# Kernel tuning notes

Hardware: AMD Instinct MI355X
Metric: run time of the kernel (lower is better)

Reference implementation:

```python
import jax, jax.numpy as jnp
import numpy as np

B, S, D, H, L = 8, 512, 1024, 16, 2
DH = D // H
EPS = 1e-6
SCALE = float(np.sqrt(DH))


def _ln(x, g, b):
    # custom LayerNormalization: unbiased std (torch default), eps added to std
    m = x.mean(axis=-1, keepdims=True)
    s = jnp.std(x, axis=-1, keepdims=True, ddof=1)
    return g * (x - m) / (s + EPS) + b


def _pos_encoding(seq_len, dim):
    pos = jnp.arange(seq_len, dtype=jnp.float32)[:, None]
    dims = jnp.arange(dim, dtype=jnp.float32)
    div = 10000.0 ** (2.0 * dims / dim)
    pe = jnp.zeros((seq_len, dim), jnp.float32)
    pe = pe.at[:, 0::2].set(jnp.sin(pos / div[0::2]))
    pe = pe.at[:, 1::2].set(jnp.cos(pos / div[1::2]))
    return pe


def setup_inputs() -> dict:
    key = jax.random.key(0)
    ks = jax.random.split(key, 20)
    std = 0.02
    p = lambda k, shape: jax.random.normal(k, shape, jnp.float32) * std
    return {
        "features": jax.random.normal(ks[0], (B, S, D), jnp.float32),
        "mask": jnp.ones((B, S), jnp.int32),
        "ln_in_g": jnp.ones((D,), jnp.float32),
        "ln_in_b": jnp.zeros((D,), jnp.float32),
        "Wq": p(ks[1], (L, D, D)), "bq": p(ks[2], (L, D)),
        "Wk": p(ks[3], (L, D, D)), "bk": p(ks[4], (L, D)),
        "Wv": p(ks[5], (L, D, D)), "bv": p(ks[6], (L, D)),
        "Wo": p(ks[7], (L, D, D)), "bo": p(ks[8], (L, D)),
        "ln1_g": jnp.ones((L, D), jnp.float32), "ln1_b": jnp.zeros((L, D), jnp.float32),
        "W1": p(ks[9], (L, D, D)), "b1": p(ks[10], (L, D)),
        "W2": p(ks[11], (L, D, D)), "b2": p(ks[12], (L, D)),
        "ln2_g": jnp.ones((L, D), jnp.float32), "ln2_b": jnp.zeros((L, D), jnp.float32),
    }


def reference(features, mask, ln_in_g, ln_in_b, Wq, bq, Wk, bk, Wv, bv, Wo, bo,
              ln1_g, ln1_b, W1, b1, W2, b2, ln2_g, ln2_b):
    # input norm + positional encoding (dropout inert at eval)
    x = _ln(features, ln_in_g, ln_in_b) + _pos_encoding(S, D)  # [B,S,D]
    # mask: positions where mask==0 are masked out with -1e18
    neg = (mask == 0)[:, None, None, :]  # [B,1,1,Sk]

    def encoder_layer(inp, i):
        q = (inp @ Wq[i].T + bq[i]).reshape(B, S, H, DH).transpose(0, 2, 1, 3)
        k = (inp @ Wk[i].T + bk[i]).reshape(B, S, H, DH).transpose(0, 2, 1, 3)
        v = (inp @ Wv[i].T + bv[i]).reshape(B, S, H, DH).transpose(0, 2, 1, 3)
        scores = jnp.einsum('bhqd,bhkd->bhqk', q, k) / SCALE
        scores = jnp.where(neg, -1e18, scores)
        attn = jax.nn.softmax(scores, axis=-1)
        ctx = jnp.einsum('bhqk,bhkd->bhqd', attn, v).transpose(0, 2, 1, 3).reshape(B, S, D)
        attn_out = ctx @ Wo[i].T + bo[i]
        s = _ln(attn_out + inp, ln1_g[i], ln1_b[i])  # residual + custom LN
        h = jax.nn.gelu(s @ W1[i].T + b1[i], approximate=False)
        f = h @ W2[i].T + b2[i]
        return _ln(f + s, ln2_g[i], ln2_b[i])

    # FAITHFUL to source: layers are NOT chained -- each layer reads the
    # original (query,key,value); output is the last layer's result.
    out = x
    for i in range(L):
        out = encoder_layer(x, i)
    return out
```

## Files before the change

kernel.cpp:

```cpp
#include <hip/hip_runtime.h>
#include <cstdint>
#include <cstddef>


typedef __attribute__((ext_vector_type(8))) short bf16x8;
typedef __attribute__((ext_vector_type(4))) short bf16x4;
typedef __attribute__((ext_vector_type(4))) float f32x4;

#define MFMA16(a, b, c) __builtin_amdgcn_mfma_f32_16x16x32_bf16((a), (b), (c), 0, 0, 0)

__device__ __forceinline__ unsigned short f2b(float f) {
  union { float f; unsigned int u; } x; x.f = f;
  unsigned int r = x.u + 0x7fffu + ((x.u >> 16) & 1u);
  return (unsigned short)(r >> 16);
}

__device__ __forceinline__ float b2f(unsigned short u) {
  union { unsigned int i; float f; } x;
  x.i = ((unsigned int)u) << 16;
  return x.f;
}

__device__ __forceinline__ void gl_lds16(const void* g, void* l) {
  __builtin_amdgcn_global_load_lds(
      (const __attribute__((address_space(1))) void*)g,
      (__attribute__((address_space(3))) void*)l, 16, 0, 0);
}

template <int BN, int EPI>
__global__ __launch_bounds__(256) void gemm_t(
    const unsigned short* __restrict__ A, const unsigned short* __restrict__ B,
    const float* __restrict__ bias, unsigned short* __restrict__ outB, int N,
    int K, int nnHalf) {
  extern __shared__ char smem[];
  char* la = smem;
  char* lb = smem + 3 * 16384;
  constexpr int NR = BN / 32;
  const int tid = threadIdx.x;
  const int l = tid & 63, w = tid >> 6;
  const int l15 = l & 15, l4 = l >> 4;
  const int xcd = blockIdx.x & 7, r = blockIdx.x >> 3;
  const int m0 = ((xcd >> 1) * 8 + (r & 7)) * 128;
  const int n0 = ((xcd & 1) * nnHalf + (r >> 3)) * BN;
  const int wr = (w >> 1) * 64, wc = (w & 1) * (BN / 2);
  const int NT = K >> 6;

#define STAGE(buf, t)                                                         \
  {                                                                           \
    const int k0_ = (t) * 64;                                                 \
    _Pragma("unroll") for (int i = 0; i < 4; ++i) {                           \
      const int c = i * 256 + tid;                                            \
      const int row = c >> 3;                                                 \
      const int gch = (c & 7) ^ (row & 7);                                    \
      gl_lds16(A + (size_t)(m0 + row) * K + k0_ + gch * 8,                    \
               la + (buf) * 16384 + (i * 256 + w * 64) * 16);                 \
    }                                                                         \
    _Pragma("unroll") for (int i = 0; i < BN / 32; ++i) {                     \
      const int c = i * 256 + tid;                                            \
      const int row = c >> 3;                                                 \
      const int gch = (c & 7) ^ (row & 7);                                    \
      gl_lds16(B + (size_t)(n0 + row) * K + k0_ + gch * 8,                    \
               lb + (buf) * (BN * 128) + (i * 256 + w * 64) * 16);            \
    }                                                                         \
  }
#define WAIT_L()                                                   \
  {                                                                \
    if constexpr (BN == 128) {                                     \
      asm volatile("s_waitcnt vmcnt(8)" ::: "memory");             \
    } else {                                                       \
      asm volatile("s_waitcnt vmcnt(6)" ::: "memory");             \
    }                                                              \
  }

  f32x4 acc[4][NR] = {};
  const int sw = l15 & 7;

  STAGE(0, 0);
  STAGE(1, 1);
  WAIT_L();
  __builtin_amdgcn_sched_barrier(0);
  __builtin_amdgcn_s_barrier();
  __builtin_amdgcn_sched_barrier(0);

  for (int t = 0; t < NT; ++t) {
    if (t + 2 < NT) {
      STAGE((t + 2) % 3, t + 2);
    }
    __builtin_amdgcn_sched_barrier(0);
    const char* abuf = la + (t % 3) * 16384;
    const char* bbuf = lb + (t % 3) * (BN * 128);
#pragma unroll
    for (int kk = 0; kk < 2; ++kk) {
      const unsigned int ch = (unsigned int)(((kk * 4 + l4) ^ sw) << 4);
      bf16x8 af[4], bfr[NR];
#pragma unroll
      for (int m = 0; m < 4; ++m)
        af[m] = *(const bf16x8*)(abuf + (wr + m * 16 + l15) * 128 + ch);
#pragma unroll
      for (int n = 0; n < NR; ++n)
        bfr[n] = *(const bf16x8*)(bbuf + (wc + n * 16 + l15) * 128 + ch);
#pragma unroll
      for (int m = 0; m < 4; ++m) {
#pragma unroll
        for (int n = 0; n < NR; ++n) {
          acc[m][n] = MFMA16(af[m], bfr[n], acc[m][n]);
        }
      }
    }
    if (t < NT - 1) {
      if (t + 2 < NT) {
        WAIT_L();
      } else {
        asm volatile("s_waitcnt vmcnt(0)" ::: "memory");
      }
      __builtin_amdgcn_sched_barrier(0);
      __builtin_amdgcn_s_barrier();
      __builtin_amdgcn_sched_barrier(0);
    }
  }
#undef STAGE
#undef WAIT_L

#pragma unroll
  for (int m = 0; m < 4; ++m) {
#pragma unroll
    for (int n = 0; n < NR; ++n) {
      const int col = n0 + wc + n * 16 + l15;
      const float bb = bias[col];
#pragma unroll
      for (int e = 0; e < 4; ++e) {
        const int row = m0 + wr + m * 16 + l4 * 4 + e;
        float v = acc[m][n][e] + bb;
        if (EPI == 1) {
          if (col < 1024) v *= 0.125f;
        } else if (EPI == 2) {
          v = 0.5f * v * (1.f + erff(v * 0.70710678118654752f));
        }
        outB[(size_t)row * N + col] = f2b(v);
      }
    }
  }
}

__global__ __launch_bounds__(256, 2) void attn_kernel(
    const unsigned short* __restrict__ qkv, const int* __restrict__ mask,
    unsigned short* __restrict__ ctx) {
  extern __shared__ char smem[];
  float* maskadd = (float*)(smem + 65536);
  const int bid = blockIdx.x;
  const int b = bid & 7, h = (bid >> 3) & 15, qt = bid >> 7;
  const int tid = threadIdx.x, l = tid & 63, w = tid >> 6;
  const int l15 = l & 15, l4 = l >> 4;
  const size_t RB = (size_t)b * 512 * 3072;

  for (int s = tid; s < 512; s += 256)
    maskadd[s] = mask[b * 512 + s] ? 0.f : -1e18f;

  const unsigned short* Kbase = qkv + RB + 1024 + h * 64;
  const unsigned short* Vbase = qkv + RB + 2048 + h * 64;

  const int kr0 = tid >> 2, kc0 = tid & 3;
  const unsigned int swzk = (unsigned int)((kr0 & 7) << 4);
  const unsigned int ka0 = ((unsigned int)(kr0 * 128 + kc0 * 16)) ^ swzk;
  const unsigned int ka1 = ((unsigned int)(kr0 * 128 + kc0 * 16 + 64)) ^ swzk;
  const int vs0 = 2 * l, vd0 = w * 16;

  bf16x8 k00, k01, k10, k11, vreg[4];
  k00 = *(const bf16x8*)(Kbase + (size_t)kr0 * 3072 + kc0 * 8);
  k01 = *(const bf16x8*)(Kbase + (size_t)kr0 * 3072 + kc0 * 8 + 32);
  k10 = *(const bf16x8*)(Kbase + (size_t)(kr0 + 64) * 3072 + kc0 * 8);
  k11 = *(const bf16x8*)(Kbase + (size_t)(kr0 + 64) * 3072 + kc0 * 8 + 32);
  vreg[0] = *(const bf16x8*)(Vbase + (size_t)vs0 * 3072 + vd0);
  vreg[1] = *(const bf16x8*)(Vbase + (size_t)vs0 * 3072 + vd0 + 8);
  vreg[2] = *(const bf16x8*)(Vbase + (size_t)(vs0 + 1) * 3072 + vd0);
  vreg[3] = *(const bf16x8*)(Vbase + (size_t)(vs0 + 1) * 3072 + vd0 + 8);

  const int q0 = qt * 64 + w * 16;
  const unsigned short* qb =
      qkv + RB + (size_t)(q0 + l15) * 3072 + h * 64 + l4 * 8;
  const bf16x8 qf0 = *(const bf16x8*)(qb);
  const bf16x8 qf1 = *(const bf16x8*)(qb + 32);

#define KWRITE(dst)                        \
  {                                        \
    *(bf16x8*)((dst) + ka0) = k00;         \
    *(bf16x8*)((dst) + ka1) = k01;         \
    *(bf16x8*)((dst) + ka0 + 8192) = k10;  \
    *(bf16x8*)((dst) + ka1 + 8192) = k11;  \
  }
#define VWRITE(dst)                                                          \
  {                                                                          \
    _Pragma("unroll") for (int j = 0; j < 16; ++j) {                         \
      const unsigned short lo_ =                                             \
          (unsigned short)((j < 8) ? vreg[0][j] : vreg[1][j - 8]);           \
      const unsigned short hi_ =                                             \
          (unsigned short)((j < 8) ? vreg[2][j] : vreg[3][j - 8]);           \
      *(unsigned int*)((dst) +                                               \
                       (((vd0 + j) * 256 + vs0 * 2) ^ ((j & 7) << 4))) =     \
          (unsigned int)lo_ | ((unsigned int)hi_ << 16);                     \
    }                                                                        \
  }

  KWRITE(smem);
  VWRITE(smem + 32768);
  __syncthreads();

  const int hi4 = l4 >> 1, gl = l4 & 1, g2 = l4 & 2;
  f32x4 acc[4] = {};
  float run_m = -1e30f, run_s = 0.f;

#pragma unroll
  for (int t = 0; t < 4; ++t) {
    char* kcur = smem + (t & 1) * 16384;
    char* vcur = smem + 32768 + (t & 1) * 16384;
    if (t < 3) {
      const int sn = (t + 1) * 128;
      k00 = *(const bf16x8*)(Kbase + (size_t)(sn + kr0) * 3072 + kc0 * 8);
      k01 = *(const bf16x8*)(Kbase + (size_t)(sn + kr0) * 3072 + kc0 * 8 + 32);
      k10 = *(const bf16x8*)(Kbase + (size_t)(sn + kr0 + 64) * 3072 + kc0 * 8);
      k11 = *(const bf16x8*)(Kbase + (size_t)(sn + kr0 + 64) * 3072 + kc0 * 8 + 32);
      vreg[0] = *(const bf16x8*)(Vbase + (size_t)(sn + vs0) * 3072 + vd0);
      vreg[1] = *(const bf16x8*)(Vbase + (size_t)(sn + vs0) * 3072 + vd0 + 8);
      vreg[2] = *(const bf16x8*)(Vbase + (size_t)(sn + vs0 + 1) * 3072 + vd0);
      vreg[3] = *(const bf16x8*)(Vbase + (size_t)(sn + vs0 + 1) * 3072 + vd0 + 8);
      __builtin_amdgcn_sched_barrier(0);
    }
    f32x4 sc[8];
    __builtin_amdgcn_s_setprio(1);
#pragma unroll
    for (int kk = 0; kk < 8; ++kk) {
      const unsigned int lin = (unsigned int)((kk * 16 + l15) * 128 + l4 * 16);
      const unsigned int swz = (unsigned int)((l15 & 7) << 4);
      const bf16x8 af0 = *(const bf16x8*)(kcur + (lin ^ swz));
      const bf16x8 af1 = *(const bf16x8*)(kcur + ((lin + 64) ^ swz));
      f32x4 c = {0.f, 0.f, 0.f, 0.f};
      c = MFMA16(af0, qf0, c);
      c = MFMA16(af1, qf1, c);
      sc[kk] = c;
    }
    __builtin_amdgcn_s_setprio(0);
    float tmx = -1e30f;
#pragma unroll
    for (int kk = 0; kk < 8; ++kk) {
#pragma unroll
      for (int e = 0; e < 4; ++e) {
        const float v = sc[kk][e] + maskadd[t * 128 + kk * 16 + l4 * 4 + e];
        sc[kk][e] = v;
        tmx = fmaxf(tmx, v);
      }
    }
    tmx = fmaxf(tmx, __shfl_xor(tmx, 16));
    tmx = fmaxf(tmx, __shfl_xor(tmx, 32));
    const float nm = (t == 0) ? tmx : fmaxf(run_m, tmx);
    float tsum = 0.f;
    unsigned int pk[8][2];
#pragma unroll
    for (int kk = 0; kk < 8; ++kk) {
      const float p0 = __expf(sc[kk][0] - nm);
      const float p1 = __expf(sc[kk][1] - nm);
      const float p2 = __expf(sc[kk][2] - nm);
      const float p3 = __expf(sc[kk][3] - nm);
      tsum += (p0 + p1) + (p2 + p3);
      asm("v_cvt_pk_bf16_f32 %0, %1, %2" : "=v"(pk[kk][0]) : "v"(p0), "v"(p1));
      asm("v_cvt_pk_bf16_f32 %0, %1, %2" : "=v"(pk[kk][1]) : "v"(p2), "v"(p3));
    }
    tsum += __shfl_xor(tsum, 16);
    tsum += __shfl_xor(tsum, 32);
    if (t == 0) {
      run_s = tsum;
    } else {
      const float scale = __expf(run_m - nm);
      run_s = run_s * scale + tsum;
      float s4[4];
#pragma unroll
      for (int e = 0; e < 4; ++e) s4[e] = __shfl(scale, l4 * 4 + e);
#pragma unroll
      for (int nt = 0; nt < 4; ++nt) {
#pragma unroll
        for (int e = 0; e < 4; ++e) acc[nt][e] *= s4[e];
      }
    }
    run_m = nm;
#pragma unroll
    for (int k2 = 0; k2 < 4; ++k2) {
      const unsigned int own0 = hi4 ? pk[2 * k2 + 1][0] : pk[2 * k2][0];
      const unsigned int own1 = hi4 ? pk[2 * k2 + 1][1] : pk[2 * k2][1];
      const unsigned int oth0 = hi4 ? pk[2 * k2][0] : pk[2 * k2 + 1][0];
      const unsigned int oth1 = hi4 ? pk[2 * k2][1] : pk[2 * k2 + 1][1];
      const unsigned int s16_0 = (unsigned int)__shfl_xor((int)own0, 16);
      const unsigned int s16_1 = (unsigned int)__shfl_xor((int)own1, 16);
      const unsigned int s32_0 = (unsigned int)__shfl_xor((int)oth0, 32);
      const unsigned int s32_1 = (unsigned int)__shfl_xor((int)oth1, 32);
      const unsigned int s48_0 = (unsigned int)__shfl_xor((int)oth0, 48);
      const unsigned int s48_1 = (unsigned int)__shfl_xor((int)oth1, 48);
      union { unsigned int u[4]; bf16x8 v; } pa;
      pa.u[0] = g2 ? (gl ? s16_0 : s32_0) : (gl ? s48_0 : own0);
      pa.u[1] = g2 ? (gl ? s16_1 : s32_1) : (gl ? s48_1 : own1);
      pa.u[2] = g2 ? (gl ? own0 : s48_0) : (gl ? s32_0 : s16_0);
      pa.u[3] = g2 ? (gl ? own1 : s48_1) : (gl ? s32_1 : s16_1);
      __builtin_amdgcn_s_setprio(1);
#pragma unroll
      for (int nt = 0; nt < 4; ++nt) {
        const int d = nt * 16 + l15;
        const unsigned int vb =
            (unsigned int)((d * 256 + k2 * 64 + l4 * 16) ^ ((l15 & 7) << 4));
        const bf16x8 vbf = *(const bf16x8*)(vcur + vb);
        acc[nt] = MFMA16(pa.v, vbf, acc[nt]);
      }
      __builtin_amdgcn_s_setprio(0);
    }
    if (t < 3) {
      char* knxt = smem + ((t + 1) & 1) * 16384;
      char* vnxt = smem + 32768 + ((t + 1) & 1) * 16384;
      KWRITE(knxt);
      VWRITE(vnxt);
      __syncthreads();
    }
  }
#undef KWRITE
#undef VWRITE

  const float inv = 1.f / run_s;
  float invq[4];
#pragma unroll
  for (int e = 0; e < 4; ++e) invq[e] = __shfl(inv, l4 * 4 + e);
#pragma unroll
  for (int nt = 0; nt < 4; ++nt) {
#pragma unroll
    for (int e = 0; e < 4; ++e) {
      const size_t row = (size_t)b * 512 + q0 + l4 * 4 + e;
      ctx[row * 1024 + h * 64 + nt * 16 + l15] = f2b(acc[nt][e] * invq[e]);
    }
  }
}

template <int MODE>
__global__ __launch_bounds__(256) void ln_k(
    const void* __restrict__ Ap, const void* __restrict__ Rp,
    const float* __restrict__ g, const float* __restrict__ bta,
    void* __restrict__ outp) {
  __shared__ float red[8];
  const int row = blockIdx.x, tid = threadIdx.x;
  const size_t base = (size_t)row * 1024 + tid * 4;
  float a4[4];
  if (MODE == 0) {
    const float4 a = *(const float4*)((const float*)Ap + base);
    a4[0] = a.x; a4[1] = a.y; a4[2] = a.z; a4[3] = a.w;
  } else {
    const bf16x4 a = *(const bf16x4*)((const unsigned short*)Ap + base);
    const bf16x4 rr = *(const bf16x4*)((const unsigned short*)Rp + base);
#pragma unroll
    for (int j = 0; j < 4; ++j)
      a4[j] = b2f((unsigned short)a[j]) + b2f((unsigned short)rr[j]);
  }
  float s = a4[0] + a4[1] + a4[2] + a4[3];
  float q = a4[0] * a4[0] + a4[1] * a4[1] + a4[2] * a4[2] + a4[3] * a4[3];
#pragma unroll
  for (int o = 32; o; o >>= 1) {
    s += __shfl_xor(s, o);
    q += __shfl_xor(q, o);
  }
  if ((tid & 63) == 0) {
    red[(tid >> 6) * 2] = s;
    red[(tid >> 6) * 2 + 1] = q;
  }
  __syncthreads();
  const float S = red[0] + red[2] + red[4] + red[6];
  const float Qs = red[1] + red[3] + red[5] + red[7];
  const float mean = S * (1.f / 1024.f);
  float var = (Qs - 1024.f * mean * mean) * (1.f / 1023.f);
  var = fmaxf(var, 0.f);
  const float inv = 1.f / (sqrtf(var) + 1e-6f);
  float o4[4];
#pragma unroll
  for (int j = 0; j < 4; ++j) {
    const int col = tid * 4 + j;
    float y = g[col] * (a4[j] - mean) * inv + bta[col];
    if (MODE == 0) {
      const float ang =
          (float)(row & 511) * exp2f((float)col * -0.025952563241307518f);
      y += (col & 1) ? cosf(ang) : sinf(ang);
    }
    o4[j] = y;
  }
  if (MODE == 2) {
    *(float4*)((float*)outp + base) = make_float4(o4[0], o4[1], o4[2], o4[3]);
  } else {
    bf16x4 pb;
    pb[0] = (short)f2b(o4[0]);
    pb[1] = (short)f2b(o4[1]);
    pb[2] = (short)f2b(o4[2]);
    pb[3] = (short)f2b(o4[3]);
    *(bf16x4*)((unsigned short*)outp + base) = pb;
  }
}

__global__ __launch_bounds__(256) void prep_weights(
    const float* __restrict__ Wq, const float* __restrict__ Wk,
    const float* __restrict__ Wv, const float* __restrict__ Wo,
    const float* __restrict__ W1, const float* __restrict__ W2,
    const float* __restrict__ bq, const float* __restrict__ bk,
    const float* __restrict__ bv, unsigned short* __restrict__ wqkv,
    unsigned short* __restrict__ wo, unsigned short* __restrict__ w1,
    unsigned short* __restrict__ w2, float* __restrict__ bqkv) {
  const int gid = blockIdx.x * 256 + threadIdx.x;
  if (gid < 1572864) {
    const int chunk = gid >> 18;
    const int off = (gid & 262143) * 4;
    const float* s;
    unsigned short* d;
    switch (chunk) {
      case 0: s = Wq; d = wqkv; break;
      case 1: s = Wk; d = wqkv + 1048576; break;
      case 2: s = Wv; d = wqkv + 2097152; break;
      case 3: s = Wo; d = wo; break;
      case 4: s = W1; d = w1; break;
      default: s = W2; d = w2; break;
    }
    const float4 v = *(const float4*)(s + off);
    bf16x4 o;
    o[0] = (short)f2b(v.x); o[1] = (short)f2b(v.y);
    o[2] = (short)f2b(v.z); o[3] = (short)f2b(v.w);
    *(bf16x4*)(d + off) = o;
  } else {
    const int idx = (gid - 1572864) * 4;
    if (idx < 3072) {
      const float* bs = idx < 1024 ? bq : (idx < 2048 ? bk - 1024 : bv - 2048);
      *(float4*)(bqkv + idx) = *(const float4*)(bs + idx);
    }
  }
}

extern "C" void kernel_launch(void* const* d_in, const int* in_sizes, int n_in,
                              void* d_out, int out_size, void* d_ws, size_t ws_size,
                              hipStream_t stream) {
  (void)in_sizes; (void)n_in; (void)out_size; (void)ws_size;
  const float* features = (const float*)d_in[0];
  const int* mask = (const int*)d_in[1];
  const float* ln_in_g = (const float*)d_in[2];
  const float* ln_in_b = (const float*)d_in[3];
  const size_t DD = 1024 * 1024;
  const float* Wq = (const float*)d_in[4] + DD;
  const float* bq = (const float*)d_in[5] + 1024;
  const float* Wk = (const float*)d_in[6] + DD;
  const float* bk = (const float*)d_in[7] + 1024;
  const float* Wv = (const float*)d_in[8] + DD;
  const float* bv = (const float*)d_in[9] + 1024;
  const float* Wo = (const float*)d_in[10] + DD;
  const float* bo = (const float*)d_in[11] + 1024;
  const float* l1g = (const float*)d_in[12] + 1024;
  const float* l1b = (const float*)d_in[13] + 1024;
  const float* W1 = (const float*)d_in[14] + DD;
  const float* b1 = (const float*)d_in[15] + 1024;
  const float* W2 = (const float*)d_in[16] + DD;
  const float* b2 = (const float*)d_in[17] + 1024;
  const float* l2g = (const float*)d_in[18] + 1024;
  const float* l2b = (const float*)d_in[19] + 1024;

  char* base = (char*)d_ws;
  unsigned short* qkv = (unsigned short*)(base);
  unsigned short* xb = (unsigned short*)(base + 25165824);
  unsigned short* ctxb = (unsigned short*)(base + 33554432);
  unsigned short* abuf = (unsigned short*)(base + 41943040);
  unsigned short* wqkv = (unsigned short*)(base + 50331648);
  unsigned short* wo = (unsigned short*)(base + 56623104);
  unsigned short* w1 = (unsigned short*)(base + 58720256);
  unsigned short* w2 = (unsigned short*)(base + 60817408);
  float* bqkv = (float*)(base + 62914560);

  hipFuncSetAttribute((const void*)gemm_t<128, 1>,
                      hipFuncAttributeMaxDynamicSharedMemorySize, 98304);
  hipFuncSetAttribute((const void*)gemm_t<64, 2>,
                      hipFuncAttributeMaxDynamicSharedMemorySize, 73728);
  hipFuncSetAttribute((const void*)gemm_t<64, 3>,
                      hipFuncAttributeMaxDynamicSharedMemorySize, 73728);
  hipFuncSetAttribute((const void*)attn_kernel,
                      hipFuncAttributeMaxDynamicSharedMemorySize, 67584);

  prep_weights<<<6147, 256, 0, stream>>>(Wq, Wk, Wv, Wo, W1, W2, bq, bk, bv,
                                         wqkv, wo, w1, w2, bqkv);
  ln_k<0><<<4096, 256, 0, stream>>>(features, nullptr, ln_in_g, ln_in_b, xb);
  gemm_t<128, 1><<<768, 256, 98304, stream>>>(xb, wqkv, bqkv, qkv, 3072, 1024, 12);
  attn_kernel<<<1024, 256, 67584, stream>>>(qkv, mask, ctxb);
  gemm_t<64, 3><<<512, 256, 73728, stream>>>(ctxb, wo, bo, abuf, 1024, 1024, 8);
  ln_k<1><<<4096, 256, 0, stream>>>(abuf, xb, l1g, l1b, ctxb);
  gemm_t<64, 2><<<512, 256, 73728, stream>>>(ctxb, w1, b1, xb, 1024, 1024, 8);
  gemm_t<64, 3><<<512, 256, 73728, stream>>>(xb, w2, b2, abuf, 1024, 1024, 8);
  ln_k<2><<<4096, 256, 0, stream>>>(abuf, ctxb, l2g, l2b, (float*)d_out);
}
```

Before: 155.0 us.

## Load GEMM B operand directly into registers, stage only A through LDS

```diff
diff --git a/kernel.cpp b/kernel.cpp
--- a/kernel.cpp
+++ b/kernel.cpp
@@ -27,25 +27,24 @@
       (__attribute__((address_space(3))) void*)l, 16, 0, 0);
 }
 
-template <int BN, int EPI>
+template <int EPI>
 __global__ __launch_bounds__(256) void gemm_t(
     const unsigned short* __restrict__ A, const unsigned short* __restrict__ B,
     const float* __restrict__ bias, unsigned short* __restrict__ outB, int N,
-    int K, int nnHalf) {
-  extern __shared__ char smem[];
-  char* la = smem;
-  char* lb = smem + 3 * 16384;
-  constexpr int NR = BN / 32;
+    int nnHalf) {
+  __shared__ char la[3 * 128 * 128];
+  constexpr int K = 1024;
+  constexpr int NT = 16;
   const int tid = threadIdx.x;
   const int l = tid & 63, w = tid >> 6;
   const int l15 = l & 15, l4 = l >> 4;
   const int xcd = blockIdx.x & 7, r = blockIdx.x >> 3;
   const int m0 = ((xcd >> 1) * 8 + (r & 7)) * 128;
-  const int n0 = ((xcd & 1) * nnHalf + (r >> 3)) * BN;
-  const int wr = (w >> 1) * 64, wc = (w & 1) * (BN / 2);
-  const int NT = K >> 6;
-
-#define STAGE(buf, t)                                                         \
+  const int n0 = ((xcd & 1) * nnHalf + (r >> 3)) * 64;
+  const int wr = (w >> 1) * 64, wc = (w & 1) * 32;
+  const int sw = l15 & 7;
+
+#define STAGE_A(buf, t)                                                       \
   {                                                                           \
     const int k0_ = (t) * 64;                                                 \
     _Pragma("unroll") for (int i = 0; i < 4; ++i) {                           \
@@ -55,61 +54,57 @@
       gl_lds16(A + (size_t)(m0 + row) * K + k0_ + gch * 8,                    \
                la + (buf) * 16384 + (i * 256 + w * 64) * 16);                 \
     }                                                                         \
-    _Pragma("unroll") for (int i = 0; i < BN / 32; ++i) {                     \
-      const int c = i * 256 + tid;                                            \
-      const int row = c >> 3;                                                 \
-      const int gch = (c & 7) ^ (row & 7);                                    \
-      gl_lds16(B + (size_t)(n0 + row) * K + k0_ + gch * 8,                    \
-               lb + (buf) * (BN * 128) + (i * 256 + w * 64) * 16);            \
+  }
+  const unsigned short* Bb = B + (size_t)(n0 + wc + l15) * K + l4 * 8;
+#define LOAD_B(pb, t)                                                         \
+  {                                                                           \
+    _Pragma("unroll") for (int kk = 0; kk < 2; ++kk) {                        \
+      _Pragma("unroll") for (int n = 0; n < 2; ++n) {                         \
+        (pb)[kk][n] =                                                         \
+            *(const bf16x8*)(Bb + (size_t)(n * 16) * K + (t) * 64 + kk * 32); \
+      }                                                                       \
     }                                                                         \
   }
-#define WAIT_L()                                                   \
-  {                                                                \
-    if constexpr (BN == 128) {                                     \
-      asm volatile("s_waitcnt vmcnt(8)" ::: "memory");             \
-    } else {                                                       \
-      asm volatile("s_waitcnt vmcnt(6)" ::: "memory");             \
-    }                                                              \
-  }
-
-  f32x4 acc[4][NR] = {};
-  const int sw = l15 & 7;
-
-  STAGE(0, 0);
-  STAGE(1, 1);
-  WAIT_L();
+
+  f32x4 acc[4][2] = {};
+  bf16x8 breg[2][2][2];
+
+  LOAD_B(breg[0], 0);
+  STAGE_A(0, 0);
+  STAGE_A(1, 1);
+  asm volatile("s_waitcnt vmcnt(4)" ::: "memory");
   __builtin_amdgcn_sched_barrier(0);
   __builtin_amdgcn_s_barrier();
   __builtin_amdgcn_sched_barrier(0);
 
+#pragma unroll
   for (int t = 0; t < NT; ++t) {
+    if (t + 1 < NT) {
+      LOAD_B(breg[(t + 1) & 1], t + 1);
+    }
     if (t + 2 < NT) {
-      STAGE((t + 2) % 3, t + 2);
+      STAGE_A((t + 2) % 3, t + 2);
     }
     __builtin_amdgcn_sched_barrier(0);
     const char* abuf = la + (t % 3) * 16384;
-    const char* bbuf = lb + (t % 3) * (BN * 128);
 #pragma unroll
     for (int kk = 0; kk < 2; ++kk) {
       const unsigned int ch = (unsigned int)(((kk * 4 + l4) ^ sw) << 4);
-      bf16x8 af[4], bfr[NR];
+      bf16x8 af[4];
 #pragma unroll
       for (int m = 0; m < 4; ++m)
         af[m] = *(const bf16x8*)(abuf + (wr + m * 16 + l15) * 128 + ch);
 #pragma unroll
-      for (int n = 0; n < NR; ++n)
-        bfr[n] = *(const bf16x8*)(bbuf + (wc + n * 16 + l15) * 128 + ch);
-#pragma unroll
       for (int m = 0; m < 4; ++m) {
 #pragma unroll
-        for (int n = 0; n < NR; ++n) {
-          acc[m][n] = MFMA16(af[m], bfr[n], acc[m][n]);
+        for (int n = 0; n < 2; ++n) {
+          acc[m][n] = MFMA16(af[m], breg[t & 1][kk][n], acc[m][n]);
         }
       }
     }
     if (t < NT - 1) {
       if (t + 2 < NT) {
-        WAIT_L();
+        asm volatile("s_waitcnt vmcnt(4)" ::: "memory");
       } else {
         asm volatile("s_waitcnt vmcnt(0)" ::: "memory");
       }
@@ -118,13 +113,13 @@
       __builtin_amdgcn_sched_barrier(0);
     }
   }
-#undef STAGE
-#undef WAIT_L
+#undef STAGE_A
+#undef LOAD_B
 
 #pragma unroll
   for (int m = 0; m < 4; ++m) {
 #pragma unroll
-    for (int n = 0; n < NR; ++n) {
+    for (int n = 0; n < 2; ++n) {
       const int col = n0 + wc + n * 16 + l15;
       const float bb = bias[col];
 #pragma unroll
@@ -468,23 +463,17 @@
   unsigned short* w2 = (unsigned short*)(base + 60817408);
   float* bqkv = (float*)(base + 62914560);
 
-  hipFuncSetAttribute((const void*)gemm_t<128, 1>,
-                      hipFuncAttributeMaxDynamicSharedMemorySize, 98304);
-  hipFuncSetAttribute((const void*)gemm_t<64, 2>,
-                      hipFuncAttributeMaxDynamicSharedMemorySize, 73728);
-  hipFuncSetAttribute((const void*)gemm_t<64, 3>,
-                      hipFuncAttributeMaxDynamicSharedMemorySize, 73728);
   hipFuncSetAttribute((const void*)attn_kernel,
                       hipFuncAttributeMaxDynamicSharedMemorySize, 67584);
 
   prep_weights<<<6147, 256, 0, stream>>>(Wq, Wk, Wv, Wo, W1, W2, bq, bk, bv,
                                          wqkv, wo, w1, w2, bqkv);
   ln_k<0><<<4096, 256, 0, stream>>>(features, nullptr, ln_in_g, ln_in_b, xb);
-  gemm_t<128, 1><<<768, 256, 98304, stream>>>(xb, wqkv, bqkv, qkv, 3072, 1024, 12);
+  gemm_t<1><<<1536, 256, 0, stream>>>(xb, wqkv, bqkv, qkv, 3072, 24);
   attn_kernel<<<1024, 256, 67584, stream>>>(qkv, mask, ctxb);
-  gemm_t<64, 3><<<512, 256, 73728, stream>>>(ctxb, wo, bo, abuf, 1024, 1024, 8);
+  gemm_t<3><<<512, 256, 0, stream>>>(ctxb, wo, bo, abuf, 1024, 8);
   ln_k<1><<<4096, 256, 0, stream>>>(abuf, xb, l1g, l1b, ctxb);
-  gemm_t<64, 2><<<512, 256, 73728, stream>>>(ctxb, w1, b1, xb, 1024, 1024, 8);
-  gemm_t<64, 3><<<512, 256, 73728, stream>>>(xb, w2, b2, abuf, 1024, 1024, 8);
+  gemm_t<2><<<512, 256, 0, stream>>>(ctxb, w1, b1, xb, 1024, 8);
+  gemm_t<3><<<512, 256, 0, stream>>>(xb, w2, b2, abuf, 1024, 8);
   ln_k<2><<<4096, 256, 0, stream>>>(abuf, ctxb, l2g, l2b, (float*)d_out);
 }
```

Result: slower. 199.9 us (+29.0%).

## Split-K the Wo and W2 GEMMs and fuse the input LayerNorm with weight prep

Applied to the files above, without the earlier changes.

```diff
diff --git a/kernel.cpp b/kernel.cpp
--- a/kernel.cpp
+++ b/kernel.cpp
@@ -30,8 +30,8 @@
 template <int BN, int EPI>
 __global__ __launch_bounds__(256) void gemm_t(
     const unsigned short* __restrict__ A, const unsigned short* __restrict__ B,
-    const float* __restrict__ bias, unsigned short* __restrict__ outB, int N,
-    int K, int nnHalf) {
+    const float* __restrict__ bias, unsigned short* __restrict__ out0,
+    unsigned short* __restrict__ out1, int N, int K, int nnHalf, int KH) {
   extern __shared__ char smem[];
   char* la = smem;
   char* lb = smem + 3 * 16384;
@@ -41,13 +41,17 @@
   const int l15 = l & 15, l4 = l >> 4;
   const int xcd = blockIdx.x & 7, r = blockIdx.x >> 3;
   const int m0 = ((xcd >> 1) * 8 + (r & 7)) * 128;
-  const int n0 = ((xcd & 1) * nnHalf + (r >> 3)) * BN;
+  const int nk = r >> 3;
+  const int nIdx = nk % nnHalf;
+  const int kh = nk / nnHalf;
+  const int n0 = ((xcd & 1) * nnHalf + nIdx) * BN;
+  const int kOff = kh * (K / KH);
   const int wr = (w >> 1) * 64, wc = (w & 1) * (BN / 2);
-  const int NT = K >> 6;
+  const int NT = (K / KH) >> 6;
 
 #define STAGE(buf, t)                                                         \
   {                                                                           \
-    const int k0_ = (t) * 64;                                                 \
+    const int k0_ = kOff + (t) * 64;                                          \
     _Pragma("unroll") for (int i = 0; i < 4; ++i) {                           \
       const int c = i * 256 + tid;                                            \
       const int row = c >> 3;                                                 \
@@ -121,12 +125,13 @@
 #undef STAGE
 #undef WAIT_L
 
+  unsigned short* outp = kh ? out1 : out0;
 #pragma unroll
   for (int m = 0; m < 4; ++m) {
 #pragma unroll
     for (int n = 0; n < NR; ++n) {
       const int col = n0 + wc + n * 16 + l15;
-      const float bb = bias[col];
+      const float bb = (kh == 0) ? bias[col] : 0.f;
 #pragma unroll
       for (int e = 0; e < 4; ++e) {
         const int row = m0 + wr + m * 16 + l4 * 4 + e;
@@ -136,7 +141,7 @@
         } else if (EPI == 2) {
           v = 0.5f * v * (1.f + erff(v * 0.70710678118654752f));
         }
-        outB[(size_t)row * N + col] = f2b(v);
+        outp[(size_t)row * N + col] = f2b(v);
       }
     }
   }
@@ -336,22 +341,21 @@
 
 template <int MODE>
 __global__ __launch_bounds__(256) void ln_k(
-    const void* __restrict__ Ap, const void* __restrict__ Rp,
-    const float* __restrict__ g, const float* __restrict__ bta,
-    void* __restrict__ outp) {
+    const unsigned short* __restrict__ A0, const unsigned short* __restrict__ A1,
+    const unsigned short* __restrict__ Rp, const float* __restrict__ g,
+    const float* __restrict__ bta, void* __restrict__ outp) {
   __shared__ float red[8];
   const int row = blockIdx.x, tid = threadIdx.x;
   const size_t base = (size_t)row * 1024 + tid * 4;
   float a4[4];
-  if (MODE == 0) {
-    const float4 a = *(const float4*)((const float*)Ap + base);
-    a4[0] = a.x; a4[1] = a.y; a4[2] = a.z; a4[3] = a.w;
-  } else {
-    const bf16x4 a = *(const bf16x4*)((const unsigned short*)Ap + base);
-    const bf16x4 rr = *(const bf16x4*)((const unsigned short*)Rp + base);
+  {
+    const bf16x4 a = *(const bf16x4*)(A0 + base);
+    const bf16x4 a2 = *(const bf16x4*)(A1 + base);
+    const bf16x4 rr = *(const bf16x4*)(Rp + base);
 #pragma unroll
     for (int j = 0; j < 4; ++j)
-      a4[j] = b2f((unsigned short)a[j]) + b2f((unsigned short)rr[j]);
+      a4[j] = b2f((unsigned short)a[j]) + b2f((unsigned short)a2[j]) +
+              b2f((unsigned short)rr[j]);
   }
   float s = a4[0] + a4[1] + a4[2] + a4[3];
   float q = a4[0] * a4[0] + a4[1] * a4[1] + a4[2] * a4[2] + a4[3] * a4[3];
@@ -371,31 +375,27 @@
   float var = (Qs - 1024.f * mean * mean) * (1.f / 1023.f);
   var = fmaxf(var, 0.f);
   const float inv = 1.f / (sqrtf(var) + 1e-6f);
-  float o4[4];
-#pragma unroll
-  for (int j = 0; j < 4; ++j) {
-    const int col = tid * 4 + j;
-    float y = g[col] * (a4[j] - mean) * inv + bta[col];
-    if (MODE == 0) {
-      const float ang =
-          (float)(row & 511) * exp2f((float)col * -0.025952563241307518f);
-      y += (col & 1) ? cosf(ang) : sinf(ang);
-    }
-    o4[j] = y;
-  }
-  if (MODE == 2) {
-    *(float4*)((float*)outp + base) = make_float4(o4[0], o4[1], o4[2], o4[3]);
+  if (MODE == 4) {
+    float4 o4;
+    o4.x = g[tid * 4 + 0] * (a4[0] - mean) * inv + bta[tid * 4 + 0];
+    o4.y = g[tid * 4 + 1] * (a4[1] - mean) * inv + bta[tid * 4 + 1];
+    o4.z = g[tid * 4 + 2] * (a4[2] - mean) * inv + bta[tid * 4 + 2];
+    o4.w = g[tid * 4 + 3] * (a4[3] - mean) * inv + bta[tid * 4 + 3];
+    *(float4*)((float*)outp + base) = o4;
   } else {
     bf16x4 pb;
-    pb[0] = (short)f2b(o4[0]);
-    pb[1] = (short)f2b(o4[1]);
-    pb[2] = (short)f2b(o4[2]);
-    pb[3] = (short)f2b(o4[3]);
+#pragma unroll
+    for (int j = 0; j < 4; ++j) {
+      const int col = tid * 4 + j;
+      pb[j] = (short)f2b(g[col] * (a4[j] - mean) * inv + bta[col]);
+    }
     *(bf16x4*)((unsigned short*)outp + base) = pb;
   }
 }
 
-__global__ __launch_bounds__(256) void prep_weights(
+__global__ __launch_bounds__(256) void prep_ln(
+    const float* __restrict__ features, const float* __restrict__ g,
+    const float* __restrict__ bta, unsigned short* __restrict__ xb,
     const float* __restrict__ Wq, const float* __restrict__ Wk,
     const float* __restrict__ Wv, const float* __restrict__ Wo,
     const float* __restrict__ W1, const float* __restrict__ W2,
@@ -403,30 +403,67 @@
     const float* __restrict__ bv, unsigned short* __restrict__ wqkv,
     unsigned short* __restrict__ wo, unsigned short* __restrict__ w1,
     unsigned short* __restrict__ w2, float* __restrict__ bqkv) {
-  const int gid = blockIdx.x * 256 + threadIdx.x;
-  if (gid < 1572864) {
-    const int chunk = gid >> 18;
-    const int off = (gid & 262143) * 4;
-    const float* s;
-    unsigned short* d;
-    switch (chunk) {
-      case 0: s = Wq; d = wqkv; break;
-      case 1: s = Wk; d = wqkv + 1048576; break;
-      case 2: s = Wv; d = wqkv + 2097152; break;
-      case 3: s = Wo; d = wo; break;
-      case 4: s = W1; d = w1; break;
-      default: s = W2; d = w2; break;
-    }
-    const float4 v = *(const float4*)(s + off);
-    bf16x4 o;
-    o[0] = (short)f2b(v.x); o[1] = (short)f2b(v.y);
-    o[2] = (short)f2b(v.z); o[3] = (short)f2b(v.w);
-    *(bf16x4*)(d + off) = o;
+  if (blockIdx.x < 4096) {
+    __shared__ float red[8];
+    const int row = blockIdx.x, tid = threadIdx.x;
+    const size_t base = (size_t)row * 1024 + tid * 4;
+    const float4 a = *(const float4*)(features + base);
+    float a4[4] = {a.x, a.y, a.z, a.w};
+    float s = a4[0] + a4[1] + a4[2] + a4[3];
+    float q = a4[0] * a4[0] + a4[1] * a4[1] + a4[2] * a4[2] + a4[3] * a4[3];
+#pragma unroll
+    for (int o = 32; o; o >>= 1) {
+      s += __shfl_xor(s, o);
+      q += __shfl_xor(q, o);
+    }
+    if ((tid & 63) == 0) {
+      red[(tid >> 6) * 2] = s;
+      red[(tid >> 6) * 2 + 1] = q;
+    }
+    __syncthreads();
+    const float S = red[0] + red[2] + red[4] + red[6];
+    const float Qs = red[1] + red[3] + red[5] + red[7];
+    const float mean = S * (1.f / 1024.f);
+    float var = (Qs - 1024.f * mean * mean) * (1.f / 1023.f);
+    var = fmaxf(var, 0.f);
+    const float inv = 1.f / (sqrtf(var) + 1e-6f);
+    bf16x4 pb;
+#pragma unroll
+    for (int j = 0; j < 4; ++j) {
+      const int col = tid * 4 + j;
+      float y = g[col] * (a4[j] - mean) * inv + bta[col];
+      const float ang =
+          (float)(row & 511) * exp2f((float)col * -0.025952563241307518f);
+      y += (col & 1) ? cosf(ang) : sinf(ang);
+      pb[j] = (short)f2b(y);
+    }
+    *(bf16x4*)(xb + base) = pb;
   } else {
-    const int idx = (gid - 1572864) * 4;
-    if (idx < 3072) {
-      const float* bs = idx < 1024 ? bq : (idx < 2048 ? bk - 1024 : bv - 2048);
-      *(float4*)(bqkv + idx) = *(const float4*)(bs + idx);
+    const int gid = (blockIdx.x - 4096) * 256 + threadIdx.x;
+    if (gid < 1572864) {
+      const int chunk = gid >> 18;
+      const int off = (gid & 262143) * 4;
+      const float* s;
+      unsigned short* d;
+      switch (chunk) {
+        case 0: s = Wq; d = wqkv; break;
+        case 1: s = Wk; d = wqkv + 1048576; break;
+        case 2: s = Wv; d = wqkv + 2097152; break;
+        case 3: s = Wo; d = wo; break;
+        case 4: s = W1; d = w1; break;
+        default: s = W2; d = w2; break;
+      }
+      const float4 v = *(const float4*)(s + off);
+      bf16x4 o;
+      o[0] = (short)f2b(v.x); o[1] = (short)f2b(v.y);
+      o[2] = (short)f2b(v.z); o[3] = (short)f2b(v.w);
+      *(bf16x4*)(d + off) = o;
+    } else {
+      const int idx = (gid - 1572864) * 4;
+      if (idx < 3072) {
+        const float* bs = idx < 1024 ? bq : (idx < 2048 ? bk - 1024 : bv - 2048);
+        *(float4*)(bqkv + idx) = *(const float4*)(bs + idx);
+      }
     }
   }
 }
@@ -461,12 +498,13 @@
   unsigned short* qkv = (unsigned short*)(base);
   unsigned short* xb = (unsigned short*)(base + 25165824);
   unsigned short* ctxb = (unsigned short*)(base + 33554432);
-  unsigned short* abuf = (unsigned short*)(base + 41943040);
-  unsigned short* wqkv = (unsigned short*)(base + 50331648);
-  unsigned short* wo = (unsigned short*)(base + 56623104);
-  unsigned short* w1 = (unsigned short*)(base + 58720256);
-  unsigned short* w2 = (unsigned short*)(base + 60817408);
-  float* bqkv = (float*)(base + 62914560);
+  unsigned short* p0 = (unsigned short*)(base + 41943040);
+  unsigned short* p1 = (unsigned short*)(base + 50331648);
+  unsigned short* wqkv = (unsigned short*)(base + 58720256);
+  unsigned short* wo = (unsigned short*)(base + 65011712);
+  unsigned short* w1 = (unsigned short*)(base + 67108864);
+  unsigned short* w2 = (unsigned short*)(base + 69206016);
+  float* bqkv = (float*)(base + 71303168);
 
   hipFuncSetAttribute((const void*)gemm_t<128, 1>,
                       hipFuncAttributeMaxDynamicSharedMemorySize, 98304);
@@ -477,14 +515,18 @@
   hipFuncSetAttribute((const void*)attn_kernel,
                       hipFuncAttributeMaxDynamicSharedMemorySize, 67584);
 
-  prep_weights<<<6147, 256, 0, stream>>>(Wq, Wk, Wv, Wo, W1, W2, bq, bk, bv,
-                                         wqkv, wo, w1, w2, bqkv);
-  ln_k<0><<<4096, 256, 0, stream>>>(features, nullptr, ln_in_g, ln_in_b, xb);
-  gemm_t<128, 1><<<768, 256, 98304, stream>>>(xb, wqkv, bqkv, qkv, 3072, 1024, 12);
+  prep_ln<<<4096 + 6147, 256, 0, stream>>>(
+      features, ln_in_g, ln_in_b, xb, Wq, Wk, Wv, Wo, W1, W2, bq, bk, bv,
+      wqkv, wo, w1, w2, bqkv);
+  gemm_t<128, 1><<<768, 256, 98304, stream>>>(xb, wqkv, bqkv, qkv, qkv, 3072,
+                                              1024, 12, 1);
   attn_kernel<<<1024, 256, 67584, stream>>>(qkv, mask, ctxb);
-  gemm_t<64, 3><<<512, 256, 73728, stream>>>(ctxb, wo, bo, abuf, 1024, 1024, 8);
-  ln_k<1><<<4096, 256, 0, stream>>>(abuf, xb, l1g, l1b, ctxb);
-  gemm_t<64, 2><<<512, 256, 73728, stream>>>(ctxb, w1, b1, xb, 1024, 1024, 8);
-  gemm_t<64, 3><<<512, 256, 73728, stream>>>(xb, w2, b2, abuf, 1024, 1024, 8);
-  ln_k<2><<<4096, 256, 0, stream>>>(abuf, ctxb, l2g, l2b, (float*)d_out);
-}
+  gemm_t<64, 3><<<1024, 256, 73728, stream>>>(ctxb, wo, bo, p0, p1, 1024, 1024,
+                                              8, 2);
+  ln_k<3><<<4096, 256, 0, stream>>>(p0, p1, xb, l1g, l1b, ctxb);
+  gemm_t<64, 2><<<512, 256, 73728, stream>>>(ctxb, w1, b1, xb, xb, 1024, 1024,
+                                             8, 1);
+  gemm_t<64, 3><<<1024, 256, 73728, stream>>>(xb, w2, b2, p0, p1, 1024, 1024,
+                                              8, 2);
+  ln_k<4><<<4096, 256, 0, stream>>>(p0, p1, ctxb, l2g, l2b, (float*)d_out);
+}
```

After: 169.7 us. 1.09x slower.
